# Optimization experiments

Measured on AMD Instinct MI355X. Metric: run time of the kernel, lower is better.

Reference implementation:

```python
import jax, jax.numpy as jnp
import numpy as np

B, S, HID, NH, HS = 4, 1024, 4096, 32, 128
ROT = 64  # rotary dim = head_size // 2 (ChatGLM partial rotary)
BLOCK_SIZE = 128


def setup_inputs() -> dict:
    key = jax.random.key(0)
    k0, k1, k2 = jax.random.split(key, 3)
    T = B * S
    hidden_states = jax.random.normal(k0, (T, HID), dtype=jnp.float32)
    w_qkv = jax.random.normal(k1, (HID, 3 * HID), dtype=jnp.float32) * 0.02
    b_qkv = jnp.zeros((3 * HID,), dtype=jnp.float32)
    w_dense = jax.random.normal(k2, (HID, HID), dtype=jnp.float32) * 0.02
    # real rotary tables: per-token position within its sequence
    inv_freq = 1.0 / (10000.0 ** (jnp.arange(0, ROT, 2, dtype=jnp.float32) / ROT))  # [ROT/2]
    pos = jnp.tile(jnp.arange(S, dtype=jnp.float32), B)  # [T]
    ang = pos[:, None] * inv_freq[None, :]  # [T, ROT/2]
    cos, sin = jnp.cos(ang), jnp.sin(ang)
    block_num = T // BLOCK_SIZE
    kv_cache_k = jnp.zeros((block_num, BLOCK_SIZE, NH, HS), dtype=jnp.float32)
    kv_cache_v = jnp.zeros((block_num, BLOCK_SIZE, NH, HS), dtype=jnp.float32)
    slots = jnp.arange(T, dtype=jnp.int32)
    return {"hidden_states": hidden_states, "cos": cos, "sin": sin,
            "w_qkv": w_qkv, "b_qkv": b_qkv, "w_dense": w_dense,
            "kv_cache_k": kv_cache_k, "kv_cache_v": kv_cache_v,
            "slots": slots, "batch": B, "seq_len": S}


def _rotary(x, cos, sin):
    # x: [T, NH, HS]; rotate-half over first ROT dims, pass-through the rest
    half = ROT // 2
    x1, x2, xp = x[..., :half], x[..., half:ROT], x[..., ROT:]
    c, s = cos[:, None, :], sin[:, None, :]
    return jnp.concatenate([x1 * c - x2 * s, x2 * c + x1 * s, xp], axis=-1)


def reference(hidden_states, cos, sin, w_qkv, b_qkv, w_dense,
              kv_cache_k, kv_cache_v, slots, batch, seq_len):
    T = hidden_states.shape[0]
    qkv = hidden_states @ w_qkv + b_qkv  # [T, 3*HID]
    q, k, v = jnp.split(qkv, 3, axis=1)
    q = q.reshape(T, NH, HS)
    k = k.reshape(T, NH, HS)
    v = v.reshape(T, NH, HS)
    q = _rotary(q, cos, sin)
    k = _rotary(k, cos, sin)
    # paged KV-cache scatter write (vectorized reshape_and_cache)
    bs = kv_cache_k.shape[1]
    bi, bo = slots // bs, slots % bs
    kv_k = kv_cache_k.at[bi, bo].set(k)
    kv_v = kv_cache_v.at[bi, bo].set(v)
    # prefill causal attention per sequence
    scale = HS ** -0.5
    q4 = q.reshape(batch, seq_len, NH, HS)
    k4 = k.reshape(batch, seq_len, NH, HS)
    v4 = v.reshape(batch, seq_len, NH, HS)
    scores = jnp.einsum("bqhd,bkhd->bhqk", q4, k4) * scale
    causal = jnp.tril(jnp.ones((seq_len, seq_len), dtype=bool))
    scores = jnp.where(causal[None, None], scores, jnp.finfo(scores.dtype).min)
    probs = jax.nn.softmax(scores, axis=-1)
    attn = jnp.einsum("bhqk,bkhd->bqhd", probs, v4).reshape(T, NH * HS)
    out = attn @ w_dense
    return out, kv_k, kv_v
```

## Files before the change

kernel.cpp:

```cpp
#include <hip/hip_runtime.h>

#define S_LEN 1024
#define NHEAD 32
#define HSZ   128
#define HIDN  4096
#define NQKV  12288
#define T_TOK 4096
#define ATT_SCALE 0.12751743f

typedef __bf16 bf16x8 __attribute__((ext_vector_type(8)));
typedef float  floatx4 __attribute__((ext_vector_type(4)));

union B8U { uint4 u; bf16x8 v; };

__device__ __forceinline__ unsigned short f2bf(float x) {
  unsigned int u = __float_as_uint(x);
  unsigned int r = (u + 0x7FFFu + ((u >> 16) & 1u)) >> 16;
  return (unsigned short)r;
}

__device__ __forceinline__ void gload_lds16(const void* g, void* l) {
  __builtin_amdgcn_global_load_lds(
      (__attribute__((address_space(1))) void*)(unsigned long long)g,
      (__attribute__((address_space(3))) void*)l, 16, 0, 0);
}

__device__ __forceinline__ bf16x8 lds_frag(const unsigned short* p) {
  return *reinterpret_cast<const bf16x8*>(p);
}

__global__ __launch_bounds__(256) void cast_bf16_kernel(
    const float* __restrict__ in, unsigned short* __restrict__ out, int n) {
  int idx = (blockIdx.x * 256 + threadIdx.x) * 4;
  if (idx >= n) return;
  float4 f = *reinterpret_cast<const float4*>(in + idx);
  ushort4 o;
  o.x = f2bf(f.x); o.y = f2bf(f.y); o.z = f2bf(f.z); o.w = f2bf(f.w);
  *reinterpret_cast<ushort4*>(out + idx) = o;
}

__global__ __launch_bounds__(256) void tcast_kernel(
    const float* __restrict__ w, unsigned short* __restrict__ wt, int K, int N) {
  __shared__ float tile[32][33];
  int n0 = blockIdx.x * 32, k0 = blockIdx.y * 32;
  int tx = threadIdx.x, ty = threadIdx.y;
#pragma unroll
  for (int i = 0; i < 32; i += 8)
    tile[ty + i][tx] = w[(size_t)(k0 + ty + i) * N + n0 + tx];
  __syncthreads();
#pragma unroll
  for (int i = 0; i < 32; i += 8)
    wt[(size_t)(n0 + ty + i) * K + k0 + tx] = f2bf(tile[tx][ty + i]);
}

__global__ __launch_bounds__(512, 2) void gemm256(
    const unsigned short* __restrict__ A, const unsigned short* __restrict__ Bt,
    const float* __restrict__ bias, float* __restrict__ C,
    int N, int K, int NBX) {
  __shared__ __align__(16) unsigned short ldsA[2][16384];
  __shared__ __align__(16) unsigned short ldsB[2][16384];

  const int tid = threadIdx.x;
  const int lane = tid & 63, w = tid >> 6;
  const int m = lane & 15, quad = lane >> 4;
  const int wm = w >> 2, wn = w & 3;

  const int nwg = gridDim.x;
  const int orig = blockIdx.x;
  const int id = (orig & 7) * (nwg >> 3) + (orig >> 3);
  const int by = id / NBX, bx = id - by * NBX;
  const int tM = by << 8, tN = bx << 8;
  const int NT = K >> 6;

  const unsigned short* pA = A + (size_t)tM * K;
  const unsigned short* pB = Bt + (size_t)tN * K;

  size_t goff0;
  {
    int o = tid * 16;
    int blk = o >> 10;
    int r = (o >> 6) & 15;
    int cB = (o & 63) ^ (((r >> 3) & 1) << 5);
    goff0 = (size_t)((blk >> 1) * 16 + r) * K + ((blk & 1) << 5) + (cB >> 1);
  }
  const size_t goff1 = goff0 + (size_t)64 * K;
  const int ldst0 = tid * 16;

  const int innerOff = (m << 6) + (((quad * 8) ^ (((m >> 3) & 1) << 4)) << 1);

  floatx4 acc[2][2][4][2] = {};

  auto STAGE = [&](int s) {
    if (s < 4 * NT) {
      const int tt = s >> 2, slot = s & 3;
      const int buf = tt & 1;
      const int half = (slot == 1 || slot == 2) ? 1 : 0;
      const unsigned short* g =
          ((slot & 1) ? pB : pA) + (size_t)(half << 7) * K + (tt << 6);
      char* l = (char*)((slot & 1) ? ldsB[buf] : ldsA[buf]) + (half << 14);
      gload_lds16(g + goff0, l + ldst0);
      gload_lds16(g + goff1, l + ldst0 + 8192);
    }
  };

  auto FRAG = [&](const unsigned short* tile, int br, int kk) -> bf16x8 {
    return *reinterpret_cast<const bf16x8*>(
        (const char*)tile + ((((br << 1) + kk) << 10) + innerOff));
  };

  auto MQ = [&](floatx4 (&ac)[4][2], bf16x8 (&aa)[4][2], bf16x8 (&bb)[2][2]) {
#pragma unroll
    for (int kk = 0; kk < 2; ++kk)
#pragma unroll
      for (int i = 0; i < 4; ++i)
#pragma unroll
        for (int j = 0; j < 2; ++j)
          ac[i][j] = __builtin_amdgcn_mfma_f32_16x16x32_bf16(
              aa[i][kk], bb[j][kk], ac[i][j], 0, 0, 0);
  };

#pragma unroll
  for (int s = 0; s < 7; ++s) STAGE(s);
  asm volatile("s_waitcnt vmcnt(6)" ::: "memory");
  __builtin_amdgcn_s_barrier();
  asm volatile("" ::: "memory");

#pragma unroll 2
  for (int t = 0; t < NT; ++t) {
    const unsigned short* lA = ldsA[t & 1];
    const unsigned short* lB = ldsB[t & 1];
    const int P = t << 2;
    bf16x8 a[4][2], b0[2][2], b1[2][2];

#pragma unroll
    for (int i = 0; i < 4; ++i) {
      a[i][0] = FRAG(lA, wm * 4 + i, 0);
      a[i][1] = FRAG(lA, wm * 4 + i, 1);
    }
#pragma unroll
    for (int j = 0; j < 2; ++j) {
      b0[j][0] = FRAG(lB, wn * 2 + j, 0);
      b0[j][1] = FRAG(lB, wn * 2 + j, 1);
    }
    STAGE(P + 7);
    __builtin_amdgcn_s_barrier();
    asm volatile("s_waitcnt lgkmcnt(0)" ::: "memory");
    __builtin_amdgcn_s_setprio(1);
    MQ(acc[0][0], a, b0);
    __builtin_amdgcn_s_setprio(0);
    __builtin_amdgcn_s_barrier();

#pragma unroll
    for (int j = 0; j < 2; ++j) {
      b1[j][0] = FRAG(lB, wn * 2 + 8 + j, 0);
      b1[j][1] = FRAG(lB, wn * 2 + 8 + j, 1);
    }
    STAGE(P + 8);
    __builtin_amdgcn_s_barrier();
    asm volatile("s_waitcnt lgkmcnt(0)" ::: "memory");
    __builtin_amdgcn_s_setprio(1);
    MQ(acc[0][1], a, b1);
    __builtin_amdgcn_s_setprio(0);
    __builtin_amdgcn_s_barrier();

#pragma unroll
    for (int i = 0; i < 4; ++i) {
      a[i][0] = FRAG(lA, wm * 4 + 8 + i, 0);
      a[i][1] = FRAG(lA, wm * 4 + 8 + i, 1);
    }
    STAGE(P + 9);
    __builtin_amdgcn_s_barrier();
    asm volatile("s_waitcnt lgkmcnt(0)" ::: "memory");
    __builtin_amdgcn_s_setprio(1);
    MQ(acc[1][1], a, b1);
    __builtin_amdgcn_s_setprio(0);
    __builtin_amdgcn_s_barrier();

#pragma unroll
    for (int j = 0; j < 2; ++j) {
      b0[j][0] = FRAG(lB, wn * 2 + j, 0);
      b0[j][1] = FRAG(lB, wn * 2 + j, 1);
    }
    STAGE(P + 10);
    __builtin_amdgcn_s_barrier();
    asm volatile("s_waitcnt lgkmcnt(0)" ::: "memory");
    __builtin_amdgcn_s_setprio(1);
    MQ(acc[1][0], a, b0);
    __builtin_amdgcn_s_setprio(0);
    if (t + 2 < NT) asm volatile("s_waitcnt vmcnt(6)" ::: "memory");
    else            asm volatile("s_waitcnt vmcnt(0)" ::: "memory");
    __builtin_amdgcn_s_barrier();
    asm volatile("" ::: "memory");
  }

#pragma unroll
  for (int rh = 0; rh < 2; ++rh)
#pragma unroll
    for (int ch = 0; ch < 2; ++ch)
#pragma unroll
      for (int i = 0; i < 4; ++i)
#pragma unroll
        for (int j = 0; j < 2; ++j) {
          const int row = tM + wm * 64 + rh * 128 + i * 16 + quad * 4;
          const int col = tN + wn * 32 + ch * 128 + j * 16 + m;
          const float bb = bias ? bias[col] : 0.0f;
          float* cp = C + (size_t)row * N + col;
#pragma unroll
          for (int rr = 0; rr < 4; ++rr)
            cp[(size_t)rr * N] = acc[rh][ch][i][j][rr] + bb;
        }
}

__global__ __launch_bounds__(256) void rope_kernel(
    const float* __restrict__ qkv, const float* __restrict__ cosb,
    const float* __restrict__ sinb, const int* __restrict__ slots,
    unsigned short* __restrict__ Qb, unsigned short* __restrict__ Kb,
    float* __restrict__ KvK, float* __restrict__ KvV) {
  const int t = blockIdx.x, tid = threadIdx.x;
  const size_t base = (size_t)t * NQKV;
  const int slot = slots[t];
  const size_t obase = (size_t)t * 4096;
  const size_t cbase = (size_t)slot * 4096;
  for (int idx = tid; idx < NHEAD * 32; idx += 256) {
    int hh = idx >> 5, r = idx & 31;
    float c = cosb[t * 32 + r], sn = sinb[t * 32 + r];
    int d0 = hh * 128 + r;
    float q1 = qkv[base + d0], q2 = qkv[base + d0 + 32];
    float k1 = qkv[base + 4096 + d0], k2 = qkv[base + 4096 + d0 + 32];
    float qr1 = q1 * c - q2 * sn, qr2 = q2 * c + q1 * sn;
    float kr1 = k1 * c - k2 * sn, kr2 = k2 * c + k1 * sn;
    Qb[obase + d0]      = f2bf(qr1 * ATT_SCALE);
    Qb[obase + d0 + 32] = f2bf(qr2 * ATT_SCALE);
    Kb[obase + d0]      = f2bf(kr1);
    Kb[obase + d0 + 32] = f2bf(kr2);
    KvK[cbase + d0] = kr1; KvK[cbase + d0 + 32] = kr2;
  }
  for (int idx = tid; idx < NHEAD * 64; idx += 256) {
    int hh = idx >> 6, p = idx & 63;
    int d = hh * 128 + 64 + p;
    float q = qkv[base + d], k = qkv[base + 4096 + d];
    Qb[obase + d] = f2bf(q * ATT_SCALE);
    Kb[obase + d] = f2bf(k);
    KvK[cbase + d] = k;
  }
  for (int idx = tid; idx < NHEAD * 128; idx += 256)
    KvV[cbase + idx] = qkv[base + 8192 + idx];
}

__global__ __launch_bounds__(256) void vtrans_kernel(
    const float* __restrict__ qkv, unsigned short* __restrict__ vt) {
  __shared__ float tile[32][33];
  int s0 = blockIdx.x * 32, d0 = blockIdx.y * 32, bh = blockIdx.z;
  int b = bh >> 5, h = bh & 31;
  int tx = threadIdx.x, ty = threadIdx.y;
#pragma unroll
  for (int i = 0; i < 32; i += 8)
    tile[ty + i][tx] =
        qkv[(size_t)(b * S_LEN + s0 + ty + i) * NQKV + 8192 + h * 128 + d0 + tx];
  __syncthreads();
#pragma unroll
  for (int i = 0; i < 32; i += 8)
    vt[(size_t)(bh * 128 + d0 + ty + i) * S_LEN + s0 + tx] = f2bf(tile[tx][ty + i]);
}

__global__ __launch_bounds__(256) void attn_kernel(
    const unsigned short* __restrict__ Q, const unsigned short* __restrict__ Kb,
    const unsigned short* __restrict__ Vt, unsigned short* __restrict__ Ob) {
  __shared__ __align__(16) unsigned short Ks[32][136];
  __shared__ __align__(16) unsigned short Vs[128][40];
  __shared__ __align__(16) unsigned short Pb[4][16][40];

  const int tid = threadIdx.x;
  const int w = tid >> 6, lane = tid & 63;
  const int m = lane & 15, quad = lane >> 4;
  const int qb = blockIdx.x, bh = blockIdx.y;
  const int b = bh >> 5, h = bh & 31;

  const int rowA = qb * 64 + w * 16 + m;
  const size_t qoff = ((size_t)(b * S_LEN + rowA)) * 4096 + h * 128;

  bf16x8 qf[4];
#pragma unroll
  for (int kc = 0; kc < 4; ++kc) {
    B8U t; t.u = *reinterpret_cast<const uint4*>(Q + qoff + kc * 32 + quad * 8);
    qf[kc] = t.v;
  }

  floatx4 O[8] = {};
  float m_run[4], l_run[4], alpha[4];
#pragma unroll
  for (int r = 0; r < 4; ++r) { m_run[r] = -3e38f; l_run[r] = 0.0f; }

  const int kend = qb * 64 + 63;
  for (int k0 = 0; k0 <= kend; k0 += 32) {
#pragma unroll
    for (int it = 0; it < 2; ++it) {
      int c = tid + it * 256;
      int key = c >> 4, d0 = (c & 15) * 8;
      uint4 val = *reinterpret_cast<const uint4*>(
          Kb + ((size_t)(b * S_LEN + k0 + key)) * 4096 + h * 128 + d0);
      *reinterpret_cast<uint4*>(&Ks[key][d0]) = val;
    }
#pragma unroll
    for (int it = 0; it < 2; ++it) {
      int c = tid + it * 256;
      int d = c >> 2, kk = (c & 3) * 8;
      uint4 val = *reinterpret_cast<const uint4*>(
          Vt + ((size_t)bh * 128 + d) * S_LEN + k0 + kk);
      *reinterpret_cast<uint4*>(&Vs[d][kk]) = val;
    }
    __syncthreads();

    floatx4 s[2];
#pragma unroll
    for (int t16 = 0; t16 < 2; ++t16) {
      floatx4 a = {};
#pragma unroll
      for (int kc = 0; kc < 4; ++kc) {
        bf16x8 kf = lds_frag(&Ks[t16 * 16 + m][kc * 32 + quad * 8]);
        a = __builtin_amdgcn_mfma_f32_16x16x32_bf16(qf[kc], kf, a, 0, 0, 0);
      }
      s[t16] = a;
    }

#pragma unroll
    for (int r = 0; r < 4; ++r) {
      int rowD = qb * 64 + w * 16 + quad * 4 + r;
      float s0 = s[0][r]; if (k0 + m > rowD)      s0 = -3e38f;
      float s1 = s[1][r]; if (k0 + 16 + m > rowD) s1 = -3e38f;
      float mx = fmaxf(s0, s1);
#pragma unroll
      for (int off = 8; off > 0; off >>= 1) mx = fmaxf(mx, __shfl_xor(mx, off));
      float mn = fmaxf(m_run[r], mx);
      float al = exp2f(m_run[r] - mn);
      float p0 = exp2f(s0 - mn), p1 = exp2f(s1 - mn);
      float rs = p0 + p1;
#pragma unroll
      for (int off = 8; off > 0; off >>= 1) rs += __shfl_xor(rs, off);
      l_run[r] = l_run[r] * al + rs;
      m_run[r] = mn; alpha[r] = al;
      Pb[w][quad * 4 + r][m]      = f2bf(p0);
      Pb[w][quad * 4 + r][16 + m] = f2bf(p1);
    }

#pragma unroll
    for (int nd = 0; nd < 8; ++nd)
#pragma unroll
      for (int r = 0; r < 4; ++r) O[nd][r] *= alpha[r];

    bf16x8 pf = lds_frag(&Pb[w][m][quad * 8]);
#pragma unroll
    for (int nd = 0; nd < 8; ++nd) {
      bf16x8 vf = lds_frag(&Vs[nd * 16 + m][quad * 8]);
      O[nd] = __builtin_amdgcn_mfma_f32_16x16x32_bf16(pf, vf, O[nd], 0, 0, 0);
    }
    __syncthreads();
  }

#pragma unroll
  for (int r = 0; r < 4; ++r) {
    int rowD = qb * 64 + w * 16 + quad * 4 + r;
    float inv = 1.0f / l_run[r];
    size_t obase = ((size_t)(b * S_LEN + rowD)) * 4096 + h * 128;
#pragma unroll
    for (int nd = 0; nd < 8; ++nd)
      Ob[obase + nd * 16 + m] = f2bf(O[nd][r] * inv);
  }
}

extern "C" void kernel_launch(void* const* d_in, const int* in_sizes, int n_in,
                              void* d_out, int out_size, void* d_ws, size_t ws_size,
                              hipStream_t stream) {
  const float* hidden  = (const float*)d_in[0];
  const float* cosb    = (const float*)d_in[1];
  const float* sinb    = (const float*)d_in[2];
  const float* w_qkv   = (const float*)d_in[3];
  const float* b_qkv   = (const float*)d_in[4];
  const float* w_dense = (const float*)d_in[5];
  const int*   slots   = (const int*)d_in[8];

  float* out = (float*)d_out;
  float* kvk = out + 16777216;
  float* kvv = out + 33554432;

  char* ws = (char*)d_ws;
  unsigned short* bfA = (unsigned short*)ws;
  unsigned short* Wt  = (unsigned short*)(ws + 33554432);
  float*          qkv = (float*)(ws + 134217728);
  unsigned short* Qb  = (unsigned short*)(ws + 335544320);
  unsigned short* Kb  = (unsigned short*)(ws + 369098752);
  unsigned short* Vt  = (unsigned short*)(ws + 402653184);

  cast_bf16_kernel<<<16384, 256, 0, stream>>>(hidden, bfA, T_TOK * HIDN);
  tcast_kernel<<<dim3(NQKV / 32, HIDN / 32), dim3(32, 8), 0, stream>>>(w_qkv, Wt, HIDN, NQKV);
  gemm256<<<dim3((T_TOK / 256) * (NQKV / 256)), 512, 0, stream>>>(
      bfA, Wt, b_qkv, qkv, NQKV, HIDN, NQKV / 256);
  rope_kernel<<<T_TOK, 256, 0, stream>>>(qkv, cosb, sinb, slots, Qb, Kb, kvk, kvv);
  vtrans_kernel<<<dim3(S_LEN / 32, HSZ / 32, 128), dim3(32, 8), 0, stream>>>(qkv, Vt);
  attn_kernel<<<dim3(S_LEN / 64, 128), 256, 0, stream>>>(Qb, Kb, Vt, bfA);
  tcast_kernel<<<dim3(HIDN / 32, HIDN / 32), dim3(32, 8), 0, stream>>>(w_dense, Wt, HIDN, HIDN);
  gemm256<<<dim3((T_TOK / 256) * (HIDN / 256)), 512, 0, stream>>>(
      bfA, Wt, nullptr, out, HIDN, HIDN, HIDN / 256);
}
```

Before: 1.317 ms.

## Software-pipeline LDS fragment loads one phase ahead of MFMA in GEMM loop

Restructures the GEMM main loop so the LDS fragment reads for the next MFMA phase are issued before the current phase's MFMAs, including prefetching the next tile's first A/B fragments across the tile boundary. This replaces the per-phase lgkmcnt(0) waits before compute. Double-buffered register sets are alternated through a manually unrolled pair of tiles, and sched_barrier keeps the compiler from reordering. The vmcnt threshold also changes. The cost is more register pressure, and the wait counts depend on subtle barrier and vmcnt correctness.

```diff
diff --git a/kernel.cpp b/kernel.cpp
--- a/kernel.cpp
+++ b/kernel.cpp
@@ -119,78 +119,72 @@
               aa[i][kk], bb[j][kk], ac[i][j], 0, 0, 0);
   };
 
+  auto LDA = [&](const unsigned short* lA, int base, bf16x8 (&a)[4][2]) {
+#pragma unroll
+    for (int i = 0; i < 4; ++i) {
+      a[i][0] = FRAG(lA, wm * 4 + base + i, 0);
+      a[i][1] = FRAG(lA, wm * 4 + base + i, 1);
+    }
+  };
+  auto LDB = [&](const unsigned short* lB, int base, bf16x8 (&b)[2][2]) {
+#pragma unroll
+    for (int j = 0; j < 2; ++j) {
+      b[j][0] = FRAG(lB, base + j, 0);
+      b[j][1] = FRAG(lB, base + j, 1);
+    }
+  };
+
+  bf16x8 a0A[4][2], b0A[2][2], a0B[4][2], b0B[2][2];
+
 #pragma unroll
   for (int s = 0; s < 7; ++s) STAGE(s);
   asm volatile("s_waitcnt vmcnt(6)" ::: "memory");
   __builtin_amdgcn_s_barrier();
   asm volatile("" ::: "memory");
-
-#pragma unroll 2
-  for (int t = 0; t < NT; ++t) {
-    const unsigned short* lA = ldsA[t & 1];
-    const unsigned short* lB = ldsB[t & 1];
+  LDA(ldsA[0], 0, a0A);
+  LDB(ldsB[0], wn * 2, b0A);
+
+  auto TILE = [&](int t, const unsigned short* lA, const unsigned short* lB,
+                  const unsigned short* lAn, const unsigned short* lBn,
+                  bf16x8 (&a0)[4][2], bf16x8 (&b0)[2][2],
+                  bf16x8 (&a0n)[4][2], bf16x8 (&b0n)[2][2]) {
+    bf16x8 a1[4][2], b1[2][2];
     const int P = t << 2;
-    bf16x8 a[4][2], b0[2][2], b1[2][2];
-
-#pragma unroll
-    for (int i = 0; i < 4; ++i) {
-      a[i][0] = FRAG(lA, wm * 4 + i, 0);
-      a[i][1] = FRAG(lA, wm * 4 + i, 1);
-    }
-#pragma unroll
-    for (int j = 0; j < 2; ++j) {
-      b0[j][0] = FRAG(lB, wn * 2 + j, 0);
-      b0[j][1] = FRAG(lB, wn * 2 + j, 1);
-    }
+    LDB(lB, wn * 2 + 8, b1);
     STAGE(P + 7);
+    __builtin_amdgcn_s_setprio(1);
+    MQ(acc[0][0], a0, b0);
+    __builtin_amdgcn_s_setprio(0);
+    __builtin_amdgcn_sched_barrier(0);
     __builtin_amdgcn_s_barrier();
-    asm volatile("s_waitcnt lgkmcnt(0)" ::: "memory");
+    LDA(lA, 8, a1);
+    STAGE(P + 8);
     __builtin_amdgcn_s_setprio(1);
-    MQ(acc[0][0], a, b0);
+    MQ(acc[0][1], a0, b1);
     __builtin_amdgcn_s_setprio(0);
+    __builtin_amdgcn_sched_barrier(0);
     __builtin_amdgcn_s_barrier();
-
-#pragma unroll
-    for (int j = 0; j < 2; ++j) {
-      b1[j][0] = FRAG(lB, wn * 2 + 8 + j, 0);
-      b1[j][1] = FRAG(lB, wn * 2 + 8 + j, 1);
-    }
-    STAGE(P + 8);
+    STAGE(P + 9);
+    __builtin_amdgcn_s_setprio(1);
+    MQ(acc[1][1], a1, b1);
+    __builtin_amdgcn_s_setprio(0);
+    if (t < NT - 2) asm volatile("s_waitcnt vmcnt(4)" ::: "memory");
+    else            asm volatile("s_waitcnt vmcnt(0)" ::: "memory");
+    __builtin_amdgcn_sched_barrier(0);
     __builtin_amdgcn_s_barrier();
-    asm volatile("s_waitcnt lgkmcnt(0)" ::: "memory");
+    if (t + 1 < NT) { LDA(lAn, 0, a0n); LDB(lBn, wn * 2, b0n); }
+    STAGE(P + 10);
     __builtin_amdgcn_s_setprio(1);
-    MQ(acc[0][1], a, b1);
+    MQ(acc[1][0], a1, b0);
     __builtin_amdgcn_s_setprio(0);
+    __builtin_amdgcn_sched_barrier(0);
     __builtin_amdgcn_s_barrier();
-
-#pragma unroll
-    for (int i = 0; i < 4; ++i) {
-      a[i][0] = FRAG(lA, wm * 4 + 8 + i, 0);
-      a[i][1] = FRAG(lA, wm * 4 + 8 + i, 1);
-    }
-    STAGE(P + 9);
-    __builtin_amdgcn_s_barrier();
-    asm volatile("s_waitcnt lgkmcnt(0)" ::: "memory");
-    __builtin_amdgcn_s_setprio(1);
-    MQ(acc[1][1], a, b1);
-    __builtin_amdgcn_s_setprio(0);
-    __builtin_amdgcn_s_barrier();
-
-#pragma unroll
-    for (int j = 0; j < 2; ++j) {
-      b0[j][0] = FRAG(lB, wn * 2 + j, 0);
-      b0[j][1] = FRAG(lB, wn * 2 + j, 1);
-    }
-    STAGE(P + 10);
-    __builtin_amdgcn_s_barrier();
-    asm volatile("s_waitcnt lgkmcnt(0)" ::: "memory");
-    __builtin_amdgcn_s_setprio(1);
-    MQ(acc[1][0], a, b0);
-    __builtin_amdgcn_s_setprio(0);
-    if (t + 2 < NT) asm volatile("s_waitcnt vmcnt(6)" ::: "memory");
-    else            asm volatile("s_waitcnt vmcnt(0)" ::: "memory");
-    __builtin_amdgcn_s_barrier();
-    asm volatile("" ::: "memory");
+  };
+
+#pragma unroll 1
+  for (int tt = 0; tt < NT; tt += 2) {
+    TILE(tt,     ldsA[0], ldsB[0], ldsA[1], ldsB[1], a0A, b0A, a0B, b0B);
+    TILE(tt + 1, ldsA[1], ldsB[1], ldsA[0], ldsB[0], a0B, b0B, a0A, b0A);
   }
 
 #pragma unroll
```

After: 3.359 ms. 2.55x slower.
